# Kernel tuning notes

Measured on AMD Instinct MI355X. Metric: run time of the kernel, lower is better.

Reference implementation:

```python
import jax, jax.numpy as jnp
import numpy as np

G = 4            # group order (e.g., C4)
H = 16           # attention heads
DH = 64          # head dim
D = 1024         # token dim = H*DH = C*G
DI = 4096        # FFN inner dim
MAXREL = 32      # relative position clamp
EPS = 1e-5


def eq_ln(x):
    # Equivariant LayerNorm: (N, D) -> (N, G, D/G), LN over last dim, no affine
    N, Dt = x.shape
    xr = x.reshape(N, G, Dt // G)
    mu = jnp.mean(xr, axis=-1, keepdims=True)
    var = jnp.var(xr, axis=-1, keepdims=True)
    return ((xr - mu) * jax.lax.rsqrt(var + EPS)).reshape(N, Dt)


def ada_ln(x, temb, w, b):
    # AdaLN: scale/shift from SiLU(temb) -> Linear -> chunk
    n = eq_ln(x)
    ss = jax.nn.silu(temb) @ w.T + b                      # (N, 2D)
    scale, shift = jnp.split(ss, 2, axis=1)
    return n * (1.0 + scale) + shift


def attention(xq, xkv, wq, wk, wv, wo, bo, rel_table):
    # xq: (B,Tq,D), xkv: (B,Tk,D); rel_table: (H, 2*MAXREL+1) or None
    B, Tq, _ = xq.shape
    Tk = xkv.shape[1]
    q = (xq @ wq.T).reshape(B, Tq, H, DH)
    k = (xkv @ wk.T).reshape(B, Tk, H, DH)
    v = (xkv @ wv.T).reshape(B, Tk, H, DH)
    scores = jnp.einsum('bthd,bkhd->bhtk', q, k) * (DH ** -0.5)
    if rel_table is not None:
        rel_idx = jnp.clip(jnp.arange(Tq)[:, None] - jnp.arange(Tk)[None, :],
                           -MAXREL, MAXREL) + MAXREL      # (Tq, Tk)
        scores = scores + rel_table[:, rel_idx][None]     # (1,H,Tq,Tk)
    attn = jax.nn.softmax(scores, axis=-1)
    out = jnp.einsum('bhtk,bkhd->bthd', attn, v).reshape(B, Tq, H * DH)
    return out @ wo.T + bo


def setup_inputs() -> dict:
    key = jax.random.key(0)
    ks = jax.random.split(key, 24)
    s = 0.02
    B, T = 4, 1024
    inp = {
        'hidden_states': jax.random.normal(ks[0], (B, T, D), jnp.float32),
        'encoder_hidden_states': jax.random.normal(ks[1], (B, T, D), jnp.float32),
        'temb': jax.random.normal(ks[2], (B * T, D), jnp.float32),
        # AdaLN 1 / 2
        'w_ada1': jax.random.normal(ks[3], (2 * D, D), jnp.float32) * s,
        'b_ada1': jnp.zeros((2 * D,), jnp.float32),
        'w_ada2': jax.random.normal(ks[4], (2 * D, D), jnp.float32) * s,
        'b_ada2': jnp.zeros((2 * D,), jnp.float32),
        # self-attention (attention_bias=False, out_bias=True)
        'wq1': jax.random.normal(ks[5], (D, D), jnp.float32) * s,
        'wk1': jax.random.normal(ks[6], (D, D), jnp.float32) * s,
        'wv1': jax.random.normal(ks[7], (D, D), jnp.float32) * s,
        'wo1': jax.random.normal(ks[8], (D, D), jnp.float32) * s,
        'bo1': jnp.zeros((D,), jnp.float32),
        'rel_bias': jax.random.normal(ks[9], (H, 2 * MAXREL + 1), jnp.float32) * s,
        # cross-attention
        'wq2': jax.random.normal(ks[10], (D, D), jnp.float32) * s,
        'wk2': jax.random.normal(ks[11], (D, D), jnp.float32) * s,
        'wv2': jax.random.normal(ks[12], (D, D), jnp.float32) * s,
        'wo2': jax.random.normal(ks[13], (D, D), jnp.float32) * s,
        'bo2': jnp.zeros((D,), jnp.float32),
        # GEGLU FFN
        'w_ff1': jax.random.normal(ks[14], (2 * DI, D), jnp.float32) * s,
        'b_ff1': jnp.zeros((2 * DI,), jnp.float32),
        'w_ff2': jax.random.normal(ks[15], (D, DI), jnp.float32) * s,
        'b_ff2': jnp.zeros((D,), jnp.float32),
    }
    return inp


def reference(hidden_states, encoder_hidden_states, temb,
              w_ada1, b_ada1, w_ada2, b_ada2,
              wq1, wk1, wv1, wo1, bo1, rel_bias,
              wq2, wk2, wv2, wo2, bo2,
              w_ff1, b_ff1, w_ff2, b_ff2):
    B, T, Dm = hidden_states.shape
    x = hidden_states.reshape(B * T, Dm)
    # 1) AdaLN + self-attention with relative position bias + residual
    x1 = ada_ln(x, temb, w_ada1, b_ada1).reshape(B, T, Dm)
    x = x + attention(x1, x1, wq1, wk1, wv1, wo1, bo1, rel_bias).reshape(B * T, Dm)
    # 2) AdaLN + cross-attention + residual
    x2 = ada_ln(x, temb, w_ada2, b_ada2).reshape(B, T, Dm)
    x = x + attention(x2, encoder_hidden_states, wq2, wk2, wv2, wo2, bo2,
                      None).reshape(B * T, Dm)
    # 3) LayerNorm + GEGLU FFN + residual
    n3 = eq_ln(x)
    h12 = n3 @ w_ff1.T + b_ff1                            # (N, 2*DI)
    a, g = jnp.split(h12, 2, axis=-1)
    ff = (a * jax.nn.gelu(g, approximate=False)) @ w_ff2.T + b_ff2
    x = x + ff
    return x.reshape(B, T, Dm)
```

## Files before the change

### kernel.cpp

```cpp
#include <hip/hip_runtime.h>
#include <math.h>

typedef __attribute__((ext_vector_type(4))) float f32x4;
typedef __attribute__((ext_vector_type(8))) __bf16 bf16x8;

#define MFMA_BF16(a, b, c) __builtin_amdgcn_mfma_f32_16x16x32_bf16((a), (b), (c), 0, 0, 0)

static __device__ __forceinline__ unsigned short f2b(float f) {
  unsigned int u = __float_as_uint(f);
  return (unsigned short)((u + 0x7FFFu + ((u >> 16) & 1u)) >> 16);
}
static __device__ __forceinline__ unsigned short bcvt(float f) {
  __bf16 h = (__bf16)f;
  return __builtin_bit_cast(unsigned short, h);
}

static __device__ __forceinline__ void gll16(const void* g, void* l) {
  __builtin_amdgcn_global_load_lds((const __attribute__((address_space(1))) void*)g,
                                   (__attribute__((address_space(3))) void*)l, 16, 0, 0);
}

__global__ __launch_bounds__(256) void f2b_kernel(const float* __restrict__ src,
                                                  unsigned short* __restrict__ dst, int n) {
  const int i = (blockIdx.x * 256 + threadIdx.x) * 4;
  if (i >= n) return;
  const float4 v = *(const float4*)(src + i);
  ushort4 o;
  o.x = f2b(v.x); o.y = f2b(v.y); o.z = f2b(v.z); o.w = f2b(v.w);
  *(ushort4*)(dst + i) = o;
}

struct CvtArgs {
  const float* src[12];
  unsigned short* dst[12];
  int start[12];
};
__global__ __launch_bounds__(256) void f2b_multi(CvtArgs a) {
  const int bid = blockIdx.x;
  int s = 11;
#pragma unroll
  for (int i = 11; i >= 1; --i)
    if (bid < a.start[i]) s = i - 1;
  const size_t i4 = (size_t)(bid - a.start[s]) * 256 + threadIdx.x;
  const float4 v = *(const float4*)(a.src[s] + i4 * 4);
  ushort4 o;
  o.x = f2b(v.x); o.y = f2b(v.y); o.z = f2b(v.z); o.w = f2b(v.w);
  *(ushort4*)(a.dst[s] + i4 * 4) = o;
}

__global__ __launch_bounds__(256) void f2bperm_kernel(const float* __restrict__ src,
                                                      unsigned short* __restrict__ dst) {
  const int r = blockIdx.x;
  const int rr = r & 4095;
  const int dr = ((rr >> 4) << 5) | ((r >> 12) << 4) | (rr & 15);
  const int c = threadIdx.x * 4;
  const float4 v = *(const float4*)(src + (size_t)r * 1024 + c);
  ushort4 o;
  o.x = f2b(v.x); o.y = f2b(v.y); o.z = f2b(v.z); o.w = f2b(v.w);
  *(ushort4*)(dst + (size_t)dr * 1024 + c) = o;
}

__global__ __launch_bounds__(256) void silu_kernel(const float* __restrict__ src,
                                                   unsigned short* __restrict__ dst, int n) {
  const int i = (blockIdx.x * 256 + threadIdx.x) * 4;
  if (i >= n) return;
  const float4 v = *(const float4*)(src + i);
  ushort4 o;
  o.x = f2b(v.x / (1.f + expf(-v.x)));
  o.y = f2b(v.y / (1.f + expf(-v.y)));
  o.z = f2b(v.z / (1.f + expf(-v.z)));
  o.w = f2b(v.w / (1.f + expf(-v.w)));
  *(ushort4*)(dst + i) = o;
}

template <int ADA>
__global__ __launch_bounds__(256) void eqln_kernel(const float* __restrict__ x,
                                                   const float* __restrict__ ss,
                                                   unsigned short* __restrict__ outp) {
  const int n = blockIdx.x;
  const int tid = threadIdx.x;
  const int g = tid >> 6, lane = tid & 63;
  const size_t base = (size_t)n * 1024 + g * 256 + lane * 4;
  const float4 v = *(const float4*)(x + base);
  float s = v.x + v.y + v.z + v.w;
  float s2 = v.x * v.x + v.y * v.y + v.z * v.z + v.w * v.w;
#pragma unroll
  for (int m = 1; m < 64; m <<= 1) {
    s += __shfl_xor(s, m, 64);
    s2 += __shfl_xor(s2, m, 64);
  }
  const float mu = s * (1.f / 256.f);
  const float var = s2 * (1.f / 256.f) - mu * mu;
  const float rs = rsqrtf(var + 1e-5f);
  float o0 = (v.x - mu) * rs, o1 = (v.y - mu) * rs, o2 = (v.z - mu) * rs, o3 = (v.w - mu) * rs;
  if (ADA) {
    const size_t sb = (size_t)n * 2048 + g * 256 + lane * 4;
    const float4 sc = *(const float4*)(ss + sb);
    const float4 sh = *(const float4*)(ss + sb + 1024);
    o0 = o0 * (1.f + sc.x) + sh.x;
    o1 = o1 * (1.f + sc.y) + sh.y;
    o2 = o2 * (1.f + sc.z) + sh.z;
    o3 = o3 * (1.f + sc.w) + sh.w;
  }
  ushort4 ov;
  ov.x = f2b(o0); ov.y = f2b(o1); ov.z = f2b(o2); ov.w = f2b(o3);
  *(ushort4*)(outp + base) = ov;
}

__global__ __launch_bounds__(256) void vtrans_kernel(const unsigned short* __restrict__ v,
                                                     unsigned short* __restrict__ vt, int T,
                                                     int ld) {
  const int t0 = blockIdx.x * 64, h = blockIdx.y, b = blockIdx.z;
  __shared__ unsigned short tile[64][65];
  const int tid = threadIdx.x;
#pragma unroll
  for (int rr = 0; rr < 2; ++rr) {
    const int tok = rr * 32 + (tid >> 3);
    const int d8 = (tid & 7) * 8;
    const uint4 x = *(const uint4*)(v + (size_t)(b * T + t0 + tok) * ld + h * 64 + d8);
    const unsigned int* xs = (const unsigned int*)&x;
#pragma unroll
    for (int j = 0; j < 4; ++j) {
      tile[d8 + 2 * j][tok] = (unsigned short)(xs[j] & 0xffffu);
      tile[d8 + 2 * j + 1][tok] = (unsigned short)(xs[j] >> 16);
    }
  }
  __syncthreads();
#pragma unroll
  for (int rr = 0; rr < 2; ++rr) {
    const int d = rr * 32 + (tid >> 3);
    const int t8 = (tid & 7) * 8;
    uint4 ov;
    unsigned int* ou = (unsigned int*)&ov;
#pragma unroll
    for (int j = 0; j < 4; ++j)
      ou[j] = (unsigned int)tile[d][t8 + 2 * j] | ((unsigned int)tile[d][t8 + 2 * j + 1] << 16);
    *(uint4*)(vt + ((size_t)((b * 16 + h) * 64 + d)) * T + t0 + t8) = ov;
  }
}

template <int BM, int BIAS, int RES, int OUTMODE>
__global__ __launch_bounds__(256, 2) void gemm_nt(const unsigned short* __restrict__ A,
                                                  const unsigned short* __restrict__ Bw,
                                                  const float* __restrict__ bias,
                                                  const float* res, void* Cout,
                                                  int M, int N, int K) {
  constexpr int MB = BM / 32;
  __shared__ unsigned short As[2][BM * 64];
  __shared__ unsigned short Bs[2][128 * 64];
  const int m0 = blockIdx.x * BM, n0 = blockIdx.y * 128;
  const int tid = threadIdx.x, lane = tid & 63;
  const int wr = (tid >> 7) & 1, wc = (tid >> 6) & 1;
  const int lr = lane & 15, ls = lane >> 4;

  const f32x4 fz = {0.f, 0.f, 0.f, 0.f};
  f32x4 acc[MB][4];
#pragma unroll
  for (int m = 0; m < MB; ++m)
#pragma unroll
    for (int n = 0; n < 4; ++n) acc[m][n] = fz;

  auto stage = [&](int buf, int k0) {
#pragma unroll
    for (int it = 0; it < BM / 32; ++it) {
      const int u = it * 256 + tid;
      const int row = u >> 3, gs = (u & 7) ^ (row & 7);
      gll16(A + (size_t)(m0 + row) * K + k0 + gs * 8, As[buf] + u * 8);
    }
#pragma unroll
    for (int it = 0; it < 4; ++it) {
      const int u = it * 256 + tid;
      const int row = u >> 3, gs = (u & 7) ^ (row & 7);
      gll16(Bw + (size_t)(n0 + row) * K + k0 + gs * 8, Bs[buf] + u * 8);
    }
  };

  stage(0, 0);
  __syncthreads();
  int cur = 0;
  for (int k0 = 0; k0 < K; k0 += 64) {
    if (k0 + 64 < K) stage(cur ^ 1, k0 + 64);
#pragma unroll
    for (int kk = 0; kk < 2; ++kk) {
      bf16x8 af[MB], bfr[4];
#pragma unroll
      for (int m = 0; m < MB; ++m) {
        const int row = wr * (BM / 2) + m * 16 + lr;
        const int slot = (kk * 4 + ls) ^ (row & 7);
        af[m] = *(const bf16x8*)(As[cur] + row * 64 + slot * 8);
      }
#pragma unroll
      for (int n = 0; n < 4; ++n) {
        const int col = wc * 64 + n * 16 + lr;
        const int slot = (kk * 4 + ls) ^ (col & 7);
        bfr[n] = *(const bf16x8*)(Bs[cur] + col * 64 + slot * 8);
      }
#pragma unroll
      for (int m = 0; m < MB; ++m)
#pragma unroll
        for (int n = 0; n < 4; ++n) acc[m][n] = MFMA_BF16(af[m], bfr[n], acc[m][n]);
    }
    __syncthreads();
    cur ^= 1;
  }

  if (OUTMODE == 2) {
    const int pn0 = n0 + wc * 64;
#pragma unroll
    for (int m = 0; m < MB; ++m) {
#pragma unroll
      for (int j = 0; j < 2; ++j) {
        const int ocol = (pn0 >> 1) + j * 16 + lr;
        const float ba = bias[ocol];
        const float bg = bias[(N >> 1) + ocol];
#pragma unroll
        for (int r = 0; r < 4; ++r) {
          const int row = m0 + wr * (BM / 2) + m * 16 + ls * 4 + r;
          const float a = acc[m][2 * j][r] + ba;
          const float g = acc[m][2 * j + 1][r] + bg;
          const float gl = 0.5f * g * (1.f + erff(g * 0.70710678118654752f));
          ((unsigned short*)Cout)[(size_t)row * (N >> 1) + ocol] = f2b(a * gl);
        }
      }
    }
    return;
  }
#pragma unroll
  for (int m = 0; m < MB; ++m) {
#pragma unroll
    for (int n = 0; n < 4; ++n) {
      const int col = n0 + wc * 64 + n * 16 + lr;
      float bv = 0.f;
      if (BIAS) bv = bias[col];
#pragma unroll
      for (int r = 0; r < 4; ++r) {
        const int row = m0 + wr * (BM / 2) + m * 16 + ls * 4 + r;
        float v = acc[m][n][r] + bv;
        if (RES) v += res[(size_t)row * N + col];
        if (OUTMODE == 1)
          ((unsigned short*)Cout)[(size_t)row * N + col] = f2b(v);
        else
          ((float*)Cout)[(size_t)row * N + col] = v;
      }
    }
  }
}

template <int RELB>
__global__ __launch_bounds__(256) void attn_kernel(const unsigned short* __restrict__ q,
                                                   const unsigned short* __restrict__ k,
                                                   const unsigned short* __restrict__ vt,
                                                   const float* __restrict__ rel,
                                                   unsigned short* __restrict__ outp,
                                                   int ldq, int ldk) {
  const int lin = blockIdx.x + (blockIdx.y << 4) + (blockIdx.z << 8);
  const int xcd = lin & 7, s = lin >> 3;
  const int g = (xcd << 3) + (s >> 4);
  const int qb = s & 15;
  const int h = g & 15, b = g >> 4;
  const int tid = threadIdx.x;
  const int wid = tid >> 6, lane = tid & 63;
  const int lr = lane & 15, ls = lane >> 4;
  const int q0 = (qb << 6) + (wid << 4);
  const float L2E = 1.44269504088896340736f;

  __shared__ unsigned short Ks[2][128 * 64];
  __shared__ unsigned short plds[4][16][64];
  __shared__ float tbl[66];

  if (RELB && tid < 65) tbl[tid] = rel[h * 65 + tid] * L2E;

  bf16x8 qa0, qa1;
  {
    const unsigned short* qp = q + (size_t)(b * 1024 + q0 + lr) * ldq + h * 64 + ls * 8;
    const bf16x8 t0 = *(const bf16x8*)qp;
    const bf16x8 t1 = *(const bf16x8*)(qp + 32);
    const float sc = 0.125f * L2E;
#pragma unroll
    for (int j = 0; j < 8; ++j) {
      qa0[j] = (__bf16)((float)t0[j] * sc);
      qa1[j] = (__bf16)((float)t1[j] * sc);
    }
  }
  bf16x8 ones;
#pragma unroll
  for (int j = 0; j < 8; ++j) ones[j] = (__bf16)1.0f;

  const f32x4 fz = {0.f, 0.f, 0.f, 0.f};
  f32x4 oacc[4];
#pragma unroll
  for (int d = 0; d < 4; ++d) oacc[d] = fz;
  f32x4 lacc = fz;

  const unsigned short* kbp = k + (size_t)(b * 1024) * ldk + h * 64;
  const unsigned short* vbp = vt + (size_t)((b * 16 + h) * 64) * 1024;

#pragma unroll
  for (int it = 0; it < 4; ++it) {
    const int u = it * 256 + tid;
    const int row = u >> 3, gs = (u & 7) ^ (row & 7);
    gll16(kbp + (size_t)row * ldk + gs * 8, Ks[0] + u * 8);
  }
  __syncthreads();

  for (int t = 0; t < 8; ++t) {
    const int kv0 = t << 7;
    bf16x8 vr[16];
#pragma unroll
    for (int hf = 0; hf < 2; ++hf)
#pragma unroll
      for (int d = 0; d < 4; ++d) {
        const unsigned short* vp = vbp + (size_t)(d * 16 + lr) * 1024 + kv0 + hf * 64 + ls * 8;
        vr[hf * 8 + 2 * d] = *(const bf16x8*)vp;
        vr[hf * 8 + 2 * d + 1] = *(const bf16x8*)(vp + 32);
      }
    if (t + 1 < 8) {
      const unsigned short* kst = kbp + (size_t)((t + 1) << 7) * ldk;
#pragma unroll
      for (int it = 0; it < 4; ++it) {
        const int u = it * 256 + tid;
        const int row = u >> 3, gs = (u & 7) ^ (row & 7);
        gll16(kst + (size_t)row * ldk + gs * 8, Ks[(t + 1) & 1] + u * 8);
      }
    }
    const unsigned short* kbuf = Ks[t & 1];
#pragma unroll
    for (int sub = 0; sub < 2; ++sub) {
      const int kvs = kv0 + sub * 64;
      f32x4 sc4[4];
      __builtin_amdgcn_s_setprio(1);
#pragma unroll
      for (int nn = 0; nn < 4; ++nn) {
        const int row = sub * 64 + nn * 16 + lr;
        const int s0 = ls ^ (row & 7), s1 = (4 + ls) ^ (row & 7);
        const bf16x8 kb0 = *(const bf16x8*)(kbuf + row * 64 + s0 * 8);
        const bf16x8 kb1 = *(const bf16x8*)(kbuf + row * 64 + s1 * 8);
        f32x4 acc = fz;
        acc = MFMA_BF16(qa0, kb0, acc);
        acc = MFMA_BF16(qa1, kb1, acc);
        sc4[nn] = acc;
      }
      __builtin_amdgcn_s_setprio(0);
      float cb = 0.f;
      bool vary = false;
      if (RELB) {
        if (kvs + 95 <= q0) {
          cb = tbl[64];
        } else if (kvs >= q0 + 47) {
          cb = tbl[0];
        } else {
          vary = true;
        }
      }
      if (vary) {
        const int bd = q0 + ls * 4 - (kvs + lr);
#pragma unroll
        for (int nn = 0; nn < 4; ++nn)
#pragma unroll
          for (int r = 0; r < 4; ++r) {
            int dl = bd + r - nn * 16;
            dl = dl < -32 ? -32 : (dl > 32 ? 32 : dl);
            const float p = __builtin_amdgcn_exp2f(fminf(sc4[nn][r] + tbl[dl + 32], 60.f));
            const int qq = ls * 4 + r;
            const int colw = ((((nn << 1) + (lr >> 3)) ^ (qq & 7)) << 3) + (lr & 7);
            plds[wid][qq][colw] = bcvt(p);
          }
      } else {
#pragma unroll
        for (int nn = 0; nn < 4; ++nn)
#pragma unroll
          for (int r = 0; r < 4; ++r) {
            const float p = __builtin_amdgcn_exp2f(fminf(sc4[nn][r] + cb, 60.f));
            const int qq = ls * 4 + r;
            const int colw = ((((nn << 1) + (lr >> 3)) ^ (qq & 7)) << 3) + (lr & 7);
            plds[wid][qq][colw] = bcvt(p);
          }
      }
      asm volatile("" ::: "memory");
      const bf16x8 pa0 = *(const bf16x8*)&plds[wid][lr][((ls ^ (lr & 7)) << 3)];
      const bf16x8 pa1 = *(const bf16x8*)&plds[wid][lr][(((4 + ls) ^ (lr & 7)) << 3)];
      __builtin_amdgcn_s_setprio(1);
      lacc = MFMA_BF16(pa0, ones, lacc);
      lacc = MFMA_BF16(pa1, ones, lacc);
#pragma unroll
      for (int d = 0; d < 4; ++d) {
        oacc[d] = MFMA_BF16(pa0, vr[sub * 8 + 2 * d], oacc[d]);
        oacc[d] = MFMA_BF16(pa1, vr[sub * 8 + 2 * d + 1], oacc[d]);
      }
      __builtin_amdgcn_s_setprio(0);
    }
    __syncthreads();
  }

  float rinv[4];
#pragma unroll
  for (int r = 0; r < 4; ++r) rinv[r] = 1.0f / lacc[r];
#pragma unroll
  for (int d = 0; d < 4; ++d)
#pragma unroll
    for (int r = 0; r < 4; ++r) {
      const float v = oacc[d][r] * rinv[r];
      outp[(size_t)(b * 1024 + q0 + ls * 4 + r) * 1024 + h * 64 + d * 16 + lr] = bcvt(v);
    }
}

extern "C" void kernel_launch(void* const* d_in, const int* in_sizes, int n_in,
                              void* d_out, int out_size, void* d_ws, size_t ws_size,
                              hipStream_t stream) {
  (void)in_sizes; (void)n_in; (void)out_size; (void)ws_size;
  const float* hs = (const float*)d_in[0];
  const float* enc = (const float*)d_in[1];
  const float* temb = (const float*)d_in[2];
  const float* wada1 = (const float*)d_in[3];
  const float* bada1 = (const float*)d_in[4];
  const float* wada2 = (const float*)d_in[5];
  const float* bada2 = (const float*)d_in[6];
  const float* wq1 = (const float*)d_in[7];
  const float* wk1 = (const float*)d_in[8];
  const float* wv1 = (const float*)d_in[9];
  const float* wo1 = (const float*)d_in[10];
  const float* bo1 = (const float*)d_in[11];
  const float* rel = (const float*)d_in[12];
  const float* wq2 = (const float*)d_in[13];
  const float* wk2 = (const float*)d_in[14];
  const float* wv2 = (const float*)d_in[15];
  const float* wo2 = (const float*)d_in[16];
  const float* bo2 = (const float*)d_in[17];
  const float* wff1 = (const float*)d_in[18];
  const float* bff1 = (const float*)d_in[19];
  const float* wff2 = (const float*)d_in[20];
  const float* bff2 = (const float*)d_in[21];
  float* out = (float*)d_out;

  char* ws = (char*)d_ws;
  const size_t MB = 1024ull * 1024ull;
  unsigned short* wb_ada1 = (unsigned short*)(ws + 0 * MB);
  unsigned short* wb_ada2 = (unsigned short*)(ws + 4 * MB);
  unsigned short* wb_q1 = (unsigned short*)(ws + 8 * MB);
  unsigned short* wb_k1 = (unsigned short*)(ws + 10 * MB);
  unsigned short* wb_v1 = (unsigned short*)(ws + 12 * MB);
  unsigned short* wb_o1 = (unsigned short*)(ws + 14 * MB);
  unsigned short* wb_q2 = (unsigned short*)(ws + 16 * MB);
  unsigned short* wb_k2 = (unsigned short*)(ws + 18 * MB);
  unsigned short* wb_v2 = (unsigned short*)(ws + 20 * MB);
  unsigned short* wb_o2 = (unsigned short*)(ws + 22 * MB);
  unsigned short* wb_ff1 = (unsigned short*)(ws + 24 * MB);
  unsigned short* wb_ff2 = (unsigned short*)(ws + 40 * MB);
  unsigned short* silu_t = (unsigned short*)(ws + 48 * MB);
  unsigned short* enc_b = (unsigned short*)(ws + 56 * MB);
  float* ssb = (float*)(ws + 64 * MB);
  unsigned short* ffin = (unsigned short*)(ws + 64 * MB);
  unsigned short* x1b = (unsigned short*)(ws + 96 * MB);
  unsigned short* qkvb = (unsigned short*)(ws + 104 * MB);
  unsigned short* qb = (unsigned short*)(ws + 104 * MB);
  unsigned short* kvb = (unsigned short*)(ws + 112 * MB);
  unsigned short* vtb = (unsigned short*)(ws + 128 * MB);
  unsigned short* aob = (unsigned short*)(ws + 136 * MB);

  const int Nrow = 4096;

  {
    CvtArgs a;
    const float* srcs[12] = {wada1, wada2, wq1, wk1, wv1, wo1, wq2, wk2, wv2, wo2, wff2, enc};
    unsigned short* dsts[12] = {wb_ada1, wb_ada2, wb_q1, wb_k1, wb_v1, wb_o1,
                                wb_q2, wb_k2, wb_v2, wb_o2, wb_ff2, enc_b};
    const int blks[12] = {2048, 2048, 1024, 1024, 1024, 1024, 1024, 1024, 1024, 1024, 4096, 4096};
    int acc = 0;
    for (int i = 0; i < 12; ++i) { a.src[i] = srcs[i]; a.dst[i] = dsts[i]; a.start[i] = acc; acc += blks[i]; }
    f2b_multi<<<acc, 256, 0, stream>>>(a);
  }
  f2bperm_kernel<<<8192, 256, 0, stream>>>(wff1, wb_ff1);
  silu_kernel<<<4096, 256, 0, stream>>>(temb, silu_t, 4096 * 1024);

  gemm_nt<128, 1, 0, 0><<<dim3(32, 16), 256, 0, stream>>>(silu_t, wb_ada1, bada1, nullptr, ssb, Nrow, 2048, 1024);
  eqln_kernel<1><<<4096, 256, 0, stream>>>(hs, ssb, x1b);
  gemm_nt<128, 0, 0, 1><<<dim3(32, 24), 256, 0, stream>>>(x1b, wb_q1, nullptr, nullptr, qkvb, Nrow, 3072, 1024);
  vtrans_kernel<<<dim3(16, 16, 4), 256, 0, stream>>>(qkvb + 2048, vtb, 1024, 3072);
  attn_kernel<1><<<dim3(16, 16, 4), 256, 0, stream>>>(qkvb, qkvb + 1024, vtb, rel, aob, 3072, 3072);
  gemm_nt<64, 1, 1, 0><<<dim3(64, 8), 256, 0, stream>>>(aob, wb_o1, bo1, hs, out, Nrow, 1024, 1024);

  gemm_nt<128, 1, 0, 0><<<dim3(32, 16), 256, 0, stream>>>(silu_t, wb_ada2, bada2, nullptr, ssb, Nrow, 2048, 1024);
  eqln_kernel<1><<<4096, 256, 0, stream>>>(out, ssb, x1b);
  gemm_nt<64, 0, 0, 1><<<dim3(64, 8), 256, 0, stream>>>(x1b, wb_q2, nullptr, nullptr, qb, Nrow, 1024, 1024);
  gemm_nt<128, 0, 0, 1><<<dim3(32, 16), 256, 0, stream>>>(enc_b, wb_k2, nullptr, nullptr, kvb, Nrow, 2048, 1024);
  vtrans_kernel<<<dim3(16, 16, 4), 256, 0, stream>>>(kvb + 1024, vtb, 1024, 2048);
  attn_kernel<0><<<dim3(16, 16, 4), 256, 0, stream>>>(qb, kvb, vtb, nullptr, aob, 1024, 2048);
  gemm_nt<64, 1, 1, 0><<<dim3(64, 8), 256, 0, stream>>>(aob, wb_o2, bo2, out, out, Nrow, 1024, 1024);

  eqln_kernel<0><<<4096, 256, 0, stream>>>(out, nullptr, x1b);
  gemm_nt<128, 1, 0, 2><<<dim3(32, 64), 256, 0, stream>>>(x1b, wb_ff1, bff1, nullptr, ffin, Nrow, 8192, 1024);
  gemm_nt<64, 1, 1, 0><<<dim3(64, 8), 256, 0, stream>>>(ffin, wb_ff2, bff2, out, out, Nrow, 1024, 4096);
}
```

Baseline: 527.4 us.

## Merge AdaLN GEMMs, store scale/shift as bf16, single-buffer GEMM with 4 blocks/CU

The two AdaLN modulation GEMMs are merged into one N=4096 GEMM over concatenated weights and biases, and its output is written as bf16 rather than fp32, halving that intermediate's traffic. The equivariant LN kernel reads the bf16 scale/shift. Separately, the GEMM drops LDS double buffering in favor of a single buffer with a sync after each load, and raises the launch bound to 4 blocks per CU. This trades load/compute overlap for occupancy, and bf16 scale/shift adds rounding error.

```diff
diff --git a/kernel.cpp b/kernel.cpp
--- a/kernel.cpp
+++ b/kernel.cpp
@@ -10,6 +10,9 @@
   unsigned int u = __float_as_uint(f);
   return (unsigned short)((u + 0x7FFFu + ((u >> 16) & 1u)) >> 16);
 }
+static __device__ __forceinline__ float b2f(unsigned short h) {
+  return __uint_as_float(((unsigned int)h) << 16);
+}
 static __device__ __forceinline__ unsigned short bcvt(float f) {
   __bf16 h = (__bf16)f;
   return __builtin_bit_cast(unsigned short, h);
@@ -18,16 +21,6 @@
 static __device__ __forceinline__ void gll16(const void* g, void* l) {
   __builtin_amdgcn_global_load_lds((const __attribute__((address_space(1))) void*)g,
                                    (__attribute__((address_space(3))) void*)l, 16, 0, 0);
-}
-
-__global__ __launch_bounds__(256) void f2b_kernel(const float* __restrict__ src,
-                                                  unsigned short* __restrict__ dst, int n) {
-  const int i = (blockIdx.x * 256 + threadIdx.x) * 4;
-  if (i >= n) return;
-  const float4 v = *(const float4*)(src + i);
-  ushort4 o;
-  o.x = f2b(v.x); o.y = f2b(v.y); o.z = f2b(v.z); o.w = f2b(v.w);
-  *(ushort4*)(dst + i) = o;
 }
 
 struct CvtArgs {
@@ -75,7 +68,7 @@
 
 template <int ADA>
 __global__ __launch_bounds__(256) void eqln_kernel(const float* __restrict__ x,
-                                                   const float* __restrict__ ss,
+                                                   const unsigned short* __restrict__ ss,
                                                    unsigned short* __restrict__ outp) {
   const int n = blockIdx.x;
   const int tid = threadIdx.x;
@@ -94,13 +87,13 @@
   const float rs = rsqrtf(var + 1e-5f);
   float o0 = (v.x - mu) * rs, o1 = (v.y - mu) * rs, o2 = (v.z - mu) * rs, o3 = (v.w - mu) * rs;
   if (ADA) {
-    const size_t sb = (size_t)n * 2048 + g * 256 + lane * 4;
-    const float4 sc = *(const float4*)(ss + sb);
-    const float4 sh = *(const float4*)(ss + sb + 1024);
-    o0 = o0 * (1.f + sc.x) + sh.x;
-    o1 = o1 * (1.f + sc.y) + sh.y;
-    o2 = o2 * (1.f + sc.z) + sh.z;
-    o3 = o3 * (1.f + sc.w) + sh.w;
+    const size_t sb = (size_t)n * 4096 + g * 256 + lane * 4;
+    const ushort4 scv = *(const ushort4*)(ss + sb);
+    const ushort4 shv = *(const ushort4*)(ss + sb + 1024);
+    o0 = o0 * (1.f + b2f(scv.x)) + b2f(shv.x);
+    o1 = o1 * (1.f + b2f(scv.y)) + b2f(shv.y);
+    o2 = o2 * (1.f + b2f(scv.z)) + b2f(shv.z);
+    o3 = o3 * (1.f + b2f(scv.w)) + b2f(shv.w);
   }
   ushort4 ov;
   ov.x = f2b(o0); ov.y = f2b(o1); ov.z = f2b(o2); ov.w = f2b(o3);
@@ -140,14 +133,14 @@
 }
 
 template <int BM, int BIAS, int RES, int OUTMODE>
-__global__ __launch_bounds__(256, 2) void gemm_nt(const unsigned short* __restrict__ A,
+__global__ __launch_bounds__(256, 4) void gemm_nt(const unsigned short* __restrict__ A,
                                                   const unsigned short* __restrict__ Bw,
                                                   const float* __restrict__ bias,
                                                   const float* res, void* Cout,
                                                   int M, int N, int K) {
   constexpr int MB = BM / 32;
-  __shared__ unsigned short As[2][BM * 64];
-  __shared__ unsigned short Bs[2][128 * 64];
+  __shared__ unsigned short As[BM * 64];
+  __shared__ unsigned short Bs[128 * 64];
   const int m0 = blockIdx.x * BM, n0 = blockIdx.y * 128;
   const int tid = threadIdx.x, lane = tid & 63;
   const int wr = (tid >> 7) & 1, wc = (tid >> 6) & 1;
@@ -160,26 +153,20 @@
 #pragma unroll
     for (int n = 0; n < 4; ++n) acc[m][n] = fz;
 
-  auto stage = [&](int buf, int k0) {
+  for (int k0 = 0; k0 < K; k0 += 64) {
 #pragma unroll
     for (int it = 0; it < BM / 32; ++it) {
       const int u = it * 256 + tid;
       const int row = u >> 3, gs = (u & 7) ^ (row & 7);
-      gll16(A + (size_t)(m0 + row) * K + k0 + gs * 8, As[buf] + u * 8);
+      gll16(A + (size_t)(m0 + row) * K + k0 + gs * 8, As + u * 8);
     }
 #pragma unroll
     for (int it = 0; it < 4; ++it) {
       const int u = it * 256 + tid;
       const int row = u >> 3, gs = (u & 7) ^ (row & 7);
-      gll16(Bw + (size_t)(n0 + row) * K + k0 + gs * 8, Bs[buf] + u * 8);
-    }
-  };
-
-  stage(0, 0);
-  __syncthreads();
-  int cur = 0;
-  for (int k0 = 0; k0 < K; k0 += 64) {
-    if (k0 + 64 < K) stage(cur ^ 1, k0 + 64);
+      gll16(Bw + (size_t)(n0 + row) * K + k0 + gs * 8, Bs + u * 8);
+    }
+    __syncthreads();
 #pragma unroll
     for (int kk = 0; kk < 2; ++kk) {
       bf16x8 af[MB], bfr[4];
@@ -187,13 +174,13 @@
       for (int m = 0; m < MB; ++m) {
         const int row = wr * (BM / 2) + m * 16 + lr;
         const int slot = (kk * 4 + ls) ^ (row & 7);
-        af[m] = *(const bf16x8*)(As[cur] + row * 64 + slot * 8);
+        af[m] = *(const bf16x8*)(As + row * 64 + slot * 8);
       }
 #pragma unroll
       for (int n = 0; n < 4; ++n) {
         const int col = wc * 64 + n * 16 + lr;
         const int slot = (kk * 4 + ls) ^ (col & 7);
-        bfr[n] = *(const bf16x8*)(Bs[cur] + col * 64 + slot * 8);
+        bfr[n] = *(const bf16x8*)(Bs + col * 64 + slot * 8);
       }
 #pragma unroll
       for (int m = 0; m < MB; ++m)
@@ -201,7 +188,6 @@
         for (int n = 0; n < 4; ++n) acc[m][n] = MFMA_BF16(af[m], bfr[n], acc[m][n]);
     }
     __syncthreads();
-    cur ^= 1;
   }
 
   if (OUTMODE == 2) {
@@ -434,8 +420,7 @@
 
   char* ws = (char*)d_ws;
   const size_t MB = 1024ull * 1024ull;
-  unsigned short* wb_ada1 = (unsigned short*)(ws + 0 * MB);
-  unsigned short* wb_ada2 = (unsigned short*)(ws + 4 * MB);
+  unsigned short* wb_ada = (unsigned short*)(ws + 0 * MB);
   unsigned short* wb_q1 = (unsigned short*)(ws + 8 * MB);
   unsigned short* wb_k1 = (unsigned short*)(ws + 10 * MB);
   unsigned short* wb_v1 = (unsigned short*)(ws + 12 * MB);
@@ -448,39 +433,42 @@
   unsigned short* wb_ff2 = (unsigned short*)(ws + 40 * MB);
   unsigned short* silu_t = (unsigned short*)(ws + 48 * MB);
   unsigned short* enc_b = (unsigned short*)(ws + 56 * MB);
-  float* ssb = (float*)(ws + 64 * MB);
+  unsigned short* ssb = (unsigned short*)(ws + 64 * MB);
   unsigned short* ffin = (unsigned short*)(ws + 64 * MB);
-  unsigned short* x1b = (unsigned short*)(ws + 96 * MB);
-  unsigned short* qkvb = (unsigned short*)(ws + 104 * MB);
-  unsigned short* qb = (unsigned short*)(ws + 104 * MB);
-  unsigned short* kvb = (unsigned short*)(ws + 112 * MB);
-  unsigned short* vtb = (unsigned short*)(ws + 128 * MB);
-  unsigned short* aob = (unsigned short*)(ws + 136 * MB);
+  float* bias_cat = (float*)(ws + 96 * MB);
+  unsigned short* x1b = (unsigned short*)(ws + 97 * MB);
+  unsigned short* qkvb = (unsigned short*)(ws + 105 * MB);
+  unsigned short* qb = (unsigned short*)(ws + 105 * MB);
+  unsigned short* kvb = (unsigned short*)(ws + 113 * MB);
+  unsigned short* vtb = (unsigned short*)(ws + 129 * MB);
+  unsigned short* aob = (unsigned short*)(ws + 137 * MB);
 
   const int Nrow = 4096;
 
   {
     CvtArgs a;
     const float* srcs[12] = {wada1, wada2, wq1, wk1, wv1, wo1, wq2, wk2, wv2, wo2, wff2, enc};
-    unsigned short* dsts[12] = {wb_ada1, wb_ada2, wb_q1, wb_k1, wb_v1, wb_o1,
+    unsigned short* dsts[12] = {wb_ada, wb_ada + 2048 * 1024, wb_q1, wb_k1, wb_v1, wb_o1,
                                 wb_q2, wb_k2, wb_v2, wb_o2, wb_ff2, enc_b};
     const int blks[12] = {2048, 2048, 1024, 1024, 1024, 1024, 1024, 1024, 1024, 1024, 4096, 4096};
     int acc = 0;
     for (int i = 0; i < 12; ++i) { a.src[i] = srcs[i]; a.dst[i] = dsts[i]; a.start[i] = acc; acc += blks[i]; }
     f2b_multi<<<acc, 256, 0, stream>>>(a);
   }
+  hipMemcpyAsync(bias_cat, bada1, 2048 * sizeof(float), hipMemcpyDeviceToDevice, stream);
+  hipMemcpyAsync(bias_cat + 2048, bada2, 2048 * sizeof(float), hipMemcpyDeviceToDevice, stream);
   f2bperm_kernel<<<8192, 256, 0, stream>>>(wff1, wb_ff1);
   silu_kernel<<<4096, 256, 0, stream>>>(temb, silu_t, 4096 * 1024);
 
-  gemm_nt<128, 1, 0, 0><<<dim3(32, 16), 256, 0, stream>>>(silu_t, wb_ada1, bada1, nullptr, ssb, Nrow, 2048, 1024);
+  gemm_nt<128, 1, 0, 1><<<dim3(32, 32), 256, 0, stream>>>(silu_t, wb_ada, bias_cat, nullptr, ssb, Nrow, 4096, 1024);
+
   eqln_kernel<1><<<4096, 256, 0, stream>>>(hs, ssb, x1b);
   gemm_nt<128, 0, 0, 1><<<dim3(32, 24), 256, 0, stream>>>(x1b, wb_q1, nullptr, nullptr, qkvb, Nrow, 3072, 1024);
   vtrans_kernel<<<dim3(16, 16, 4), 256, 0, stream>>>(qkvb + 2048, vtb, 1024, 3072);
   attn_kernel<1><<<dim3(16, 16, 4), 256, 0, stream>>>(qkvb, qkvb + 1024, vtb, rel, aob, 3072, 3072);
   gemm_nt<64, 1, 1, 0><<<dim3(64, 8), 256, 0, stream>>>(aob, wb_o1, bo1, hs, out, Nrow, 1024, 1024);
 
-  gemm_nt<128, 1, 0, 0><<<dim3(32, 16), 256, 0, stream>>>(silu_t, wb_ada2, bada2, nullptr, ssb, Nrow, 2048, 1024);
-  eqln_kernel<1><<<4096, 256, 0, stream>>>(out, ssb, x1b);
+  eqln_kernel<1><<<4096, 256, 0, stream>>>(out, ssb + 2048, x1b);
   gemm_nt<64, 0, 0, 1><<<dim3(64, 8), 256, 0, stream>>>(x1b, wb_q2, nullptr, nullptr, qb, Nrow, 1024, 1024);
   gemm_nt<128, 0, 0, 1><<<dim3(32, 16), 256, 0, stream>>>(enc_b, wb_k2, nullptr, nullptr, kvb, Nrow, 2048, 1024);
   vtrans_kernel<<<dim3(16, 16, 4), 256, 0, stream>>>(kvb + 1024, vtb, 1024, 2048);
```

Measured after the change: 486.1 us. 7.8% less time.
